# Kernel optimization log

Measured on AMD Instinct MI355X. Metric: run time of the kernel, lower is better.

Reference implementation:

```python
import jax, jax.numpy as jnp
import numpy as np

B, T, C = 4, 2048, 1024
H, HD = 16, 64  # n_head, head_size; H*HD == C


def setup_inputs() -> dict:
    key = jax.random.key(0)
    ks = jax.random.split(key, 5)
    scale = 1.0 / np.sqrt(C)
    return {
        "x": jax.random.normal(ks[0], (B, T, C), dtype=jnp.float32),
        "Wq": jax.random.normal(ks[1], (C, C), dtype=jnp.float32) * scale,
        "Wk": jax.random.normal(ks[2], (C, C), dtype=jnp.float32) * scale,
        "Wv": jax.random.normal(ks[3], (C, C), dtype=jnp.float32) * scale,
        "Wo": jax.random.normal(ks[4], (C, C), dtype=jnp.float32) * scale,
    }


def reference(x, Wq, Wk, Wv, Wo):
    # Linear projections (torch nn.Linear: y = x @ W.T), split into heads.
    def heads(W):
        return (x @ W.T).reshape(B, T, H, HD).transpose(0, 2, 1, 3)  # [B,H,T,HD]

    q, k, v = heads(Wq), heads(Wk), heads(Wv)
    # scaled dot-product scores: [B,H,T,T]
    wei = jnp.einsum("bhqd,bhkd->bhqk", q, k) * (HD ** -0.5)
    causal = jnp.tril(jnp.ones((T, T), dtype=bool))
    wei = jnp.where(causal, wei, -jnp.inf)
    wei = jax.nn.softmax(wei, axis=-1)
    out = jnp.einsum("bhqk,bhkd->bhqd", wei, v)  # [B,H,T,HD]
    out = out.transpose(0, 2, 1, 3).reshape(B, T, C)
    return out @ Wo.T
```

## Files before the change

kernel.cpp:

```cpp
#include <hip/hip_runtime.h>

#define TT 2048
#define CC 1024
#define HH 16
#define HD 64

typedef __bf16 bf16x8 __attribute__((ext_vector_type(8)));
typedef float f32x4 __attribute__((ext_vector_type(4)));

using as1_cvoid = __attribute__((address_space(1))) const void;
using as3_void  = __attribute__((address_space(3))) void;

__device__ __forceinline__ unsigned short f2bf(float f) {
  __bf16 b = (__bf16)f;
  return __builtin_bit_cast(unsigned short, b);
}

__device__ __forceinline__ void gload_lds16(const void* g, void* l) {
  __builtin_amdgcn_global_load_lds((as1_cvoid*)g, (as3_void*)l, 16, 0, 0);
}

__global__ void castk(const float* __restrict__ s, unsigned short* __restrict__ d, int n) {
  int i = (blockIdx.x * blockDim.x + threadIdx.x) * 4;
  if (i < n) {
    float4 v = *reinterpret_cast<const float4*>(s + i);
    ushort4 o;
    o.x = f2bf(v.x); o.y = f2bf(v.y); o.z = f2bf(v.z); o.w = f2bf(v.w);
    *reinterpret_cast<ushort4*>(d + i) = o;
  }
}

#define BM 128
#define BN 128
#define BK 64

__device__ __forceinline__ void stage128x64(const unsigned short* __restrict__ src,
                                            int ld, char* ldsbase, int tid) {
#pragma unroll
  for (int it = 0; it < 4; ++it) {
    int j = it * 256 + tid;
    int row = j >> 3;
    int lg = (j & 7) ^ (row & 7);
    const unsigned short* g = src + row * ld + lg * 8;
    gload_lds16(g, ldsbase + j * 16);
  }
}

template <int OUTF32>
__global__ __launch_bounds__(256)
void gemm_bt(const unsigned short* __restrict__ A, const unsigned short* __restrict__ B,
             void* __restrict__ Cout, int M, int N, int K) {
  __shared__ char lds[2][2 * BM * BK * 2];
  const int tid = threadIdx.x;
  const int lane = tid & 63;
  const int w = tid >> 6;
  const int wr = w >> 1, wc = w & 1;
  const int l15 = lane & 15, l4 = lane >> 4;

  const int rowA0 = blockIdx.x * BM;
  const int colB0 = blockIdx.y * BN;

  f32x4 acc[4][4] = {};

  const unsigned short* Abase = A + (size_t)rowA0 * K;
  const unsigned short* Bbase = B + (size_t)colB0 * K;

  int a_off[2][4], b_off[2][4];
#pragma unroll
  for (int kk = 0; kk < 2; ++kk)
#pragma unroll
    for (int m = 0; m < 4; ++m) {
      int row = wr * 64 + m * 16 + l15;
      int g = kk * 4 + l4;
      a_off[kk][m] = row * 128 + ((g ^ (row & 7)) * 16);
      int rowb = wc * 64 + m * 16 + l15;
      b_off[kk][m] = rowb * 128 + ((g ^ (rowb & 7)) * 16);
    }

  const int NT = K / BK;
  stage128x64(Abase, K, &lds[0][0], tid);
  stage128x64(Bbase, K, &lds[0][BM * BK * 2], tid);
  asm volatile("s_waitcnt vmcnt(0)" ::: "memory");
  __syncthreads();

  int buf = 0;
  for (int t = 0; t < NT; ++t) {
    if (t + 1 < NT) {
      stage128x64(Abase + (t + 1) * BK, K, &lds[buf ^ 1][0], tid);
      stage128x64(Bbase + (t + 1) * BK, K, &lds[buf ^ 1][BM * BK * 2], tid);
    }
    const char* aLds = &lds[buf][0];
    const char* bLds = &lds[buf][BM * BK * 2];
#pragma unroll
    for (int kk = 0; kk < 2; ++kk) {
      bf16x8 af[4], bfv[4];
#pragma unroll
      for (int m = 0; m < 4; ++m) af[m] = *reinterpret_cast<const bf16x8*>(aLds + a_off[kk][m]);
#pragma unroll
      for (int n = 0; n < 4; ++n) bfv[n] = *reinterpret_cast<const bf16x8*>(bLds + b_off[kk][n]);
#pragma unroll
      for (int m = 0; m < 4; ++m)
#pragma unroll
        for (int n = 0; n < 4; ++n)
          acc[m][n] = __builtin_amdgcn_mfma_f32_16x16x32_bf16(af[m], bfv[n], acc[m][n], 0, 0, 0);
    }
    asm volatile("s_waitcnt vmcnt(0)" ::: "memory");
    __syncthreads();
    buf ^= 1;
  }

#pragma unroll
  for (int m = 0; m < 4; ++m) {
#pragma unroll
    for (int r = 0; r < 4; ++r) {
      int row = rowA0 + wr * 64 + m * 16 + l4 * 4 + r;
#pragma unroll
      for (int n = 0; n < 4; ++n) {
        int col = colB0 + wc * 64 + n * 16 + l15;
        if (OUTF32)
          reinterpret_cast<float*>(Cout)[(size_t)row * N + col] = acc[m][n][r];
        else
          reinterpret_cast<unsigned short*>(Cout)[(size_t)row * N + col] = f2bf(acc[m][n][r]);
      }
    }
  }
}

__global__ __launch_bounds__(256)
void attn(const unsigned short* __restrict__ Q, const unsigned short* __restrict__ Kmat,
          const unsigned short* __restrict__ V, unsigned short* __restrict__ O) {
  __shared__ char smem[24576];
  const int tid = threadIdx.x, lane = tid & 63, w = tid >> 6;
  const int l15 = lane & 15, l4 = lane >> 4;
  const int i = blockIdx.x;
  const int bh = blockIdx.y;
  const int b = bh >> 4, h = bh & 15;
  const size_t bT = (size_t)b * TT;
  const int q0A = i * 64 + w * 16;
  const int q0B = (31 - i) * 64 + w * 16;
  const int lastA = i;
  const int lastB = 31 - i;

  char* Ks = smem;
  char* VsL = smem + 8192;
  char* Pw = smem + 16384 + w * 2048;

  const unsigned short* qpA = Q + (bT + q0A + l15) * CC + h * HD;
  const unsigned short* qpB = Q + (bT + q0B + l15) * CC + h * HD;
  bf16x8 qfA[2], qfB[2];
  qfA[0] = *reinterpret_cast<const bf16x8*>(qpA + l4 * 8);
  qfA[1] = *reinterpret_cast<const bf16x8*>(qpA + 32 + l4 * 8);
  qfB[0] = *reinterpret_cast<const bf16x8*>(qpB + l4 * 8);
  qfB[1] = *reinterpret_cast<const bf16x8*>(qpB + 32 + l4 * 8);

  f32x4 oA[4] = {}, oB[4] = {};
  float mA[4], lA[4], mB[4], lB[4];
#pragma unroll
  for (int r = 0; r < 4; ++r) {
    mA[r] = -1e30f; lA[r] = 0.f; mB[r] = -1e30f; lB[r] = 0.f;
  }

  int koff[4][2], voff[4][2], poff[2];
#pragma unroll
  for (int n = 0; n < 4; ++n)
#pragma unroll
    for (int kk = 0; kk < 2; ++kk) {
      int row = n * 16 + l15;
      int g = kk * 4 + l4;
      koff[n][kk] = row * 128 + ((g ^ (row & 7)) * 16);
      voff[n][kk] = row * 128 + ((g ^ (row & 7) ^ ((row >> 3) & 7)) * 16);
    }
#pragma unroll
  for (int kk = 0; kk < 2; ++kk) {
    int row = l15;
    int g = kk * 4 + l4;
    poff[kk] = row * 128 + ((g ^ (row & 7)) * 16);
  }

  const float sc = 0.125f;
  const float LOG2E = 1.44269504f;

#define TILE_BODY(QF, OO, MR, LR, Q0, ISDIAG, KB0)                               \
  {                                                                              \
    f32x4 s_[4] = {};                                                            \
    _Pragma("unroll")                                                            \
    for (int n = 0; n < 4; ++n)                                                  \
      _Pragma("unroll")                                                          \
      for (int kk = 0; kk < 2; ++kk) {                                           \
        bf16x8 kf = *reinterpret_cast<const bf16x8*>(Ks + koff[n][kk]);          \
        s_[n] = __builtin_amdgcn_mfma_f32_16x16x32_bf16(QF[kk], kf, s_[n], 0, 0, 0); \
      }                                                                          \
    if (ISDIAG) {                                                                \
      _Pragma("unroll")                                                          \
      for (int n = 0; n < 4; ++n) {                                              \
        int key = (KB0) + n * 16 + l15;                                          \
        _Pragma("unroll")                                                        \
        for (int r = 0; r < 4; ++r) {                                            \
          int q = (Q0) + l4 * 4 + r;                                             \
          if (key > q) s_[n][r] = -1e30f;                                        \
        }                                                                        \
      }                                                                          \
    }                                                                            \
    float tm_[4];                                                                \
    _Pragma("unroll")                                                            \
    for (int r = 0; r < 4; ++r)                                                  \
      tm_[r] = fmaxf(fmaxf(s_[0][r], s_[1][r]), fmaxf(s_[2][r], s_[3][r]));      \
    _Pragma("unroll")                                                            \
    for (int off = 1; off < 16; off <<= 1)                                       \
      _Pragma("unroll")                                                          \
      for (int r = 0; r < 4; ++r) tm_[r] = fmaxf(tm_[r], __shfl_xor(tm_[r], off, 64)); \
    float mnew_[4], alpha_[4];                                                   \
    _Pragma("unroll")                                                            \
    for (int r = 0; r < 4; ++r) {                                                \
      mnew_[r] = fmaxf(MR[r], tm_[r] * sc);                                      \
      alpha_[r] = exp2f((MR[r] - mnew_[r]) * LOG2E);                             \
      MR[r] = mnew_[r];                                                          \
    }                                                                            \
    float ts_[4] = {0.f, 0.f, 0.f, 0.f};                                         \
    _Pragma("unroll")                                                            \
    for (int n = 0; n < 4; ++n)                                                  \
      _Pragma("unroll")                                                          \
      for (int r = 0; r < 4; ++r) {                                              \
        float p = exp2f((s_[n][r] * sc - mnew_[r]) * LOG2E);                     \
        s_[n][r] = p;                                                            \
        ts_[r] += p;                                                             \
      }                                                                          \
    _Pragma("unroll")                                                            \
    for (int off = 1; off < 16; off <<= 1)                                       \
      _Pragma("unroll")                                                          \
      for (int r = 0; r < 4; ++r) ts_[r] += __shfl_xor(ts_[r], off, 64);         \
    _Pragma("unroll")                                                            \
    for (int r = 0; r < 4; ++r) LR[r] = LR[r] * alpha_[r] + ts_[r];              \
    _Pragma("unroll")                                                            \
    for (int nf2 = 0; nf2 < 4; ++nf2)                                            \
      _Pragma("unroll")                                                          \
      for (int r = 0; r < 4; ++r) OO[nf2][r] *= alpha_[r];                       \
    _Pragma("unroll")                                                            \
    for (int n = 0; n < 4; ++n)                                                  \
      _Pragma("unroll")                                                          \
      for (int r = 0; r < 4; ++r) {                                              \
        int row = l4 * 4 + r;                                                    \
        int col = n * 16 + l15;                                                  \
        int gq = col >> 3;                                                       \
        int off = row * 128 + ((gq ^ (row & 7)) * 16) + (col & 7) * 2;           \
        *reinterpret_cast<__bf16*>(Pw + off) = (__bf16)s_[n][r];                 \
      }                                                                          \
    asm volatile("s_waitcnt lgkmcnt(0)" ::: "memory");                           \
    __builtin_amdgcn_sched_barrier(0);                                           \
    _Pragma("unroll")                                                            \
    for (int kk = 0; kk < 2; ++kk) {                                             \
      bf16x8 pf = *reinterpret_cast<const bf16x8*>(Pw + poff[kk]);               \
      _Pragma("unroll")                                                          \
      for (int nf2 = 0; nf2 < 4; ++nf2) {                                        \
        bf16x8 vf = *reinterpret_cast<const bf16x8*>(VsL + voff[nf2][kk]);       \
        OO[nf2] = __builtin_amdgcn_mfma_f32_16x16x32_bf16(pf, vf, OO[nf2], 0, 0, 0); \
      }                                                                          \
    }                                                                            \
  }

  for (int t = 0; t <= lastB; ++t) {
    const int kb0 = t * 64;
    __syncthreads();
#pragma unroll
    for (int it = 0; it < 2; ++it) {
      int j = it * 256 + tid;
      int row = j >> 3;
      int lg = (j & 7) ^ (row & 7);
      const unsigned short* g = Kmat + (bT + kb0 + row) * CC + h * HD + lg * 8;
      gload_lds16(g, Ks + j * 16);
    }
#pragma unroll
    for (int it = 0; it < 2; ++it) {
      int j = it * 256 + tid;
      int key = j >> 3;
      int d0 = (j & 7) * 8;
      bf16x8 vv = *reinterpret_cast<const bf16x8*>(V + (bT + kb0 + key) * CC + h * HD + d0);
#pragma unroll
      for (int jj = 0; jj < 8; ++jj) {
        int row = d0 + jj;
        int gq = key >> 3;
        int off = row * 128 + ((gq ^ (row & 7) ^ ((row >> 3) & 7)) * 16) + (key & 7) * 2;
        *reinterpret_cast<__bf16*>(VsL + off) = vv[jj];
      }
    }
    asm volatile("s_waitcnt vmcnt(0)" ::: "memory");
    __syncthreads();

    if (t <= lastA) {
      TILE_BODY(qfA, oA, mA, lA, q0A, (t == lastA), kb0)
    }
    TILE_BODY(qfB, oB, mB, lB, q0B, (t == lastB), kb0)
  }
#undef TILE_BODY

#pragma unroll
  for (int nf2 = 0; nf2 < 4; ++nf2)
#pragma unroll
    for (int r = 0; r < 4; ++r) {
      int col = h * HD + nf2 * 16 + l15;
      int qA = q0A + l4 * 4 + r;
      O[(bT + qA) * CC + col] = f2bf(oA[nf2][r] / lA[r]);
      int qB = q0B + l4 * 4 + r;
      O[(bT + qB) * CC + col] = f2bf(oB[nf2][r] / lB[r]);
    }
}

extern "C" void kernel_launch(void* const* d_in, const int* in_sizes, int n_in,
                              void* d_out, int out_size, void* d_ws, size_t ws_size,
                              hipStream_t stream) {
  const float* x  = (const float*)d_in[0];
  const float* Wq = (const float*)d_in[1];
  const float* Wk = (const float*)d_in[2];
  const float* Wv = (const float*)d_in[3];
  const float* Wo = (const float*)d_in[4];

  char* ws = (char*)d_ws;
  const size_t NX = (size_t)4 * TT * CC;
  const size_t NW = (size_t)CC * CC;
  unsigned short* xb  = (unsigned short*)(ws);
  unsigned short* qb  = (unsigned short*)(ws + 1 * NX * 2);
  unsigned short* kb  = (unsigned short*)(ws + 2 * NX * 2);
  unsigned short* vb  = (unsigned short*)(ws + 3 * NX * 2);
  unsigned short* ob  = (unsigned short*)(ws + 4 * NX * 2);
  unsigned short* wqb = (unsigned short*)(ws + 5 * NX * 2);
  unsigned short* wkb = (unsigned short*)(ws + 5 * NX * 2 + 1 * NW * 2);
  unsigned short* wvb = (unsigned short*)(ws + 5 * NX * 2 + 2 * NW * 2);
  unsigned short* wob = (unsigned short*)(ws + 5 * NX * 2 + 3 * NW * 2);

  castk<<<(int)(NX / 1024), 256, 0, stream>>>(x, xb, (int)NX);
  castk<<<(int)(NW / 1024), 256, 0, stream>>>(Wq, wqb, (int)NW);
  castk<<<(int)(NW / 1024), 256, 0, stream>>>(Wk, wkb, (int)NW);
  castk<<<(int)(NW / 1024), 256, 0, stream>>>(Wv, wvb, (int)NW);
  castk<<<(int)(NW / 1024), 256, 0, stream>>>(Wo, wob, (int)NW);

  dim3 gg(8192 / BM, CC / BN);
  gemm_bt<0><<<gg, 256, 0, stream>>>(xb, wqb, qb, 8192, CC, CC);
  gemm_bt<0><<<gg, 256, 0, stream>>>(xb, wkb, kb, 8192, CC, CC);
  gemm_bt<0><<<gg, 256, 0, stream>>>(xb, wvb, vb, 8192, CC, CC);

  attn<<<dim3(16, 4 * HH), 256, 0, stream>>>(qb, kb, vb, ob);

  gemm_bt<1><<<gg, 256, 0, stream>>>(ob, wob, d_out, 8192, CC, CC);
}
```

Measured before the change: 364.1 us.

## Double-buffer K tiles and prefetch V into registers during attention compute

Restructures the attention main loop so the next K tile is loaded into an alternate LDS buffer asynchronously, and the next V tile is held in registers while the current tile is computed. The transposed V write to LDS happens after compute. This hides global-load latency behind MFMA work. It also folds the softmax scale and log2e into one constant to save a multiply per element, and raises LDS use and adds a min-blocks launch bound, which may constrain registers.

```diff
diff --git a/kernel.cpp b/kernel.cpp
--- a/kernel.cpp
+++ b/kernel.cpp
@@ -126,10 +126,10 @@
   }
 }
 
-__global__ __launch_bounds__(256)
+__global__ __launch_bounds__(256, 4)
 void attn(const unsigned short* __restrict__ Q, const unsigned short* __restrict__ Kmat,
           const unsigned short* __restrict__ V, unsigned short* __restrict__ O) {
-  __shared__ char smem[24576];
+  __shared__ char smem[32768];
   const int tid = threadIdx.x, lane = tid & 63, w = tid >> 6;
   const int l15 = lane & 15, l4 = lane >> 4;
   const int i = blockIdx.x;
@@ -141,9 +141,8 @@
   const int lastA = i;
   const int lastB = 31 - i;
 
-  char* Ks = smem;
-  char* VsL = smem + 8192;
-  char* Pw = smem + 16384 + w * 2048;
+  char* VsL = smem + 16384;
+  char* Pw = smem + 24576 + w * 2048;
 
   const unsigned short* qpA = Q + (bT + q0A + l15) * CC + h * HD;
   const unsigned short* qpB = Q + (bT + q0B + l15) * CC + h * HD;
@@ -177,8 +176,39 @@
     poff[kk] = row * 128 + ((g ^ (row & 7)) * 16);
   }
 
-  const float sc = 0.125f;
-  const float LOG2E = 1.44269504f;
+  const float sc2 = 0.125f * 1.44269504f;
+  bf16x8 vreg[2];
+
+#define STAGE_K(KB0, DST)                                                        \
+  _Pragma("unroll")                                                              \
+  for (int it = 0; it < 2; ++it) {                                               \
+    int j = it * 256 + tid;                                                      \
+    int row = j >> 3;                                                            \
+    int lg = (j & 7) ^ (row & 7);                                                \
+    gload_lds16(Kmat + (bT + (KB0) + row) * CC + h * HD + lg * 8, (DST) + j * 16); \
+  }
+#define LOAD_V(KB0)                                                              \
+  _Pragma("unroll")                                                              \
+  for (int it = 0; it < 2; ++it) {                                               \
+    int j = it * 256 + tid;                                                      \
+    int key = j >> 3;                                                            \
+    int d0 = (j & 7) * 8;                                                        \
+    vreg[it] = *reinterpret_cast<const bf16x8*>(V + (bT + (KB0) + key) * CC + h * HD + d0); \
+  }
+#define WRITE_V()                                                                \
+  _Pragma("unroll")                                                              \
+  for (int it = 0; it < 2; ++it) {                                               \
+    int j = it * 256 + tid;                                                      \
+    int key = j >> 3;                                                            \
+    int d0 = (j & 7) * 8;                                                        \
+    _Pragma("unroll")                                                            \
+    for (int jj = 0; jj < 8; ++jj) {                                             \
+      int row = d0 + jj;                                                         \
+      int gq = key >> 3;                                                         \
+      int off = row * 128 + ((gq ^ (row & 7) ^ ((row >> 3) & 7)) * 16) + (key & 7) * 2; \
+      *reinterpret_cast<__bf16*>(VsL + off) = vreg[it][jj];                      \
+    }                                                                            \
+  }
 
 #define TILE_BODY(QF, OO, MR, LR, Q0, ISDIAG, KB0)                               \
   {                                                                              \
@@ -212,8 +242,8 @@
     float mnew_[4], alpha_[4];                                                   \
     _Pragma("unroll")                                                            \
     for (int r = 0; r < 4; ++r) {                                                \
-      mnew_[r] = fmaxf(MR[r], tm_[r] * sc);                                      \
-      alpha_[r] = exp2f((MR[r] - mnew_[r]) * LOG2E);                             \
+      mnew_[r] = fmaxf(MR[r], tm_[r] * sc2);                                     \
+      alpha_[r] = exp2f(MR[r] - mnew_[r]);                                       \
       MR[r] = mnew_[r];                                                          \
     }                                                                            \
     float ts_[4] = {0.f, 0.f, 0.f, 0.f};                                         \
@@ -221,7 +251,7 @@
     for (int n = 0; n < 4; ++n)                                                  \
       _Pragma("unroll")                                                          \
       for (int r = 0; r < 4; ++r) {                                              \
-        float p = exp2f((s_[n][r] * sc - mnew_[r]) * LOG2E);                     \
+        float p = exp2f(s_[n][r] * sc2 - mnew_[r]);                              \
         s_[n][r] = p;                                                            \
         ts_[r] += p;                                                             \
       }                                                                          \
@@ -258,40 +288,39 @@
     }                                                                            \
   }
 
+  STAGE_K(0, smem)
+  LOAD_V(0)
+  asm volatile("s_waitcnt vmcnt(0)" ::: "memory");
+  WRITE_V()
+  __syncthreads();
+
+  int buf = 0;
   for (int t = 0; t <= lastB; ++t) {
     const int kb0 = t * 64;
-    __syncthreads();
-#pragma unroll
-    for (int it = 0; it < 2; ++it) {
-      int j = it * 256 + tid;
-      int row = j >> 3;
-      int lg = (j & 7) ^ (row & 7);
-      const unsigned short* g = Kmat + (bT + kb0 + row) * CC + h * HD + lg * 8;
-      gload_lds16(g, Ks + j * 16);
-    }
-#pragma unroll
-    for (int it = 0; it < 2; ++it) {
-      int j = it * 256 + tid;
-      int key = j >> 3;
-      int d0 = (j & 7) * 8;
-      bf16x8 vv = *reinterpret_cast<const bf16x8*>(V + (bT + kb0 + key) * CC + h * HD + d0);
-#pragma unroll
-      for (int jj = 0; jj < 8; ++jj) {
-        int row = d0 + jj;
-        int gq = key >> 3;
-        int off = row * 128 + ((gq ^ (row & 7) ^ ((row >> 3) & 7)) * 16) + (key & 7) * 2;
-        *reinterpret_cast<__bf16*>(VsL + off) = vv[jj];
-      }
-    }
-    asm volatile("s_waitcnt vmcnt(0)" ::: "memory");
-    __syncthreads();
+    if (t < lastB) {
+      char* kDst = smem + (buf ^ 1) * 8192;
+      STAGE_K(kb0 + 64, kDst)
+      LOAD_V(kb0 + 64)
+    }
+    const char* Ks = smem + buf * 8192;
 
     if (t <= lastA) {
       TILE_BODY(qfA, oA, mA, lA, q0A, (t == lastA), kb0)
     }
     TILE_BODY(qfB, oB, mB, lB, q0B, (t == lastB), kb0)
+
+    __syncthreads();
+    if (t < lastB) {
+      asm volatile("s_waitcnt vmcnt(0)" ::: "memory");
+      WRITE_V()
+      __syncthreads();
+    }
+    buf ^= 1;
   }
 #undef TILE_BODY
+#undef STAGE_K
+#undef LOAD_V
+#undef WRITE_V
 
 #pragma unroll
   for (int nf2 = 0; nf2 < 4; ++nf2)
```

After: 688.3 us. 1.89x slower.
